# Performance work log

Hardware: AMD Instinct MI355X
Metric: run time of the kernel (lower is better)

The kernel has to match this reference:

```python
import jax, jax.numpy as jnp
import numpy as np
from jax import lax

N_FFT = 1024
HOP = 256
FFT_BIN = N_FFT // 2 + 1  # 513


def make_stft_kernel(n_fft: int) -> jnp.ndarray:
    """Fixed DFT basis kernel, shape (2*fft_bin, 1, n_fft), windowed with periodic Hann."""
    fft_bin = n_fft // 2 + 1
    # torch.linspace(0, 1, n_fft) is endpoint-inclusive, same as jnp.linspace
    t = jnp.linspace(0.0, 1.0, n_fft, dtype=jnp.float32)[None, None, :]
    k = jnp.arange(fft_bin, dtype=jnp.float32)[:, None, None]
    xt = t * k * (2.0 * jnp.pi)
    kernel = jnp.concatenate([jnp.cos(xt), jnp.sin(xt)], axis=0)  # (2*fft_bin, 1, n_fft)
    # torch.hann_window is periodic: 0.5*(1 - cos(2*pi*n/N))
    n = jnp.arange(n_fft, dtype=jnp.float32)
    hann = 0.5 * (1.0 - jnp.cos(2.0 * jnp.pi * n / n_fft))
    return kernel * hann[None, None, :]


def setup_inputs() -> dict:
    key = jax.random.key(0)
    x = jax.random.normal(key, (16, 1, 262144), dtype=jnp.float32)
    kernel = make_stft_kernel(N_FFT)
    return {"x": x, "kernel": kernel}


def reference(x, kernel):
    # padding == 'center'
    left = N_FFT // 2
    right = N_FFT - left
    x = jnp.pad(x, ((0, 0), (0, 0), (left, right)))
    # strided conv1d with fixed DFT-basis kernel
    y = lax.conv_general_dilated(
        x, kernel,
        window_strides=(HOP,),
        padding='VALID',
        dimension_numbers=('NCW', 'OIW', 'NCW'),
    )  # (B, 2*fft_bin, num_frames)
    real, imag = jnp.split(y, 2, axis=1)
    return real, imag
```

## Files before the change

### kernel.cpp

```cpp
#include <hip/hip_runtime.h>
#include <hip/hip_bf16.h>

#define NFFT    1024
#define HOPSZ   256
#define XLEN    262144
#define PADLEN  (XLEN + NFFT)
#define NBATCH  16
#define NBINS2  1026
#define FBIN    513
#define NFRAMES 1025
#define NGF     (NBATCH * NFRAMES)
#define TOTOUT  ((size_t)NBATCH * FBIN * NFRAMES)

#define KT 64
#define NKT 16
#define NT_TILES 64
#define MT_TILES 4
#define NWG (MT_TILES * NT_TILES)
#define ABYTES 32768
#define BUFE   32768
#define BUFB   65536
#define NTAIL  49184
#define PSTRIDE 132
#define LDS_BYTES (256 * PSTRIDE * 4)

typedef short bf16x8 __attribute__((ext_vector_type(8)));
typedef float f32x4  __attribute__((ext_vector_type(4)));
typedef unsigned short u16x8 __attribute__((ext_vector_type(8)));
typedef unsigned short u16x4 __attribute__((ext_vector_type(4)));

__device__ __forceinline__ unsigned short f2bf(float f) {
  union { float f; unsigned u; } v; v.f = f;
  unsigned r = v.u + 0x7fffu + ((v.u >> 16) & 1u);
  return (unsigned short)(r >> 16);
}
__device__ __forceinline__ float bf2f(unsigned short h) {
  union { unsigned u; float f; } v; v.u = ((unsigned)h) << 16; return v.f;
}

typedef __attribute__((address_space(1))) void void_g;
typedef __attribute__((address_space(3))) void void_l;
__device__ __forceinline__ void gload_lds16(const void* g, void* l) {
  __builtin_amdgcn_global_load_lds((void_g*)(g), (void_l*)(l), 16, 0, 0);
}

__global__ __launch_bounds__(256) void pack_x_kernel(const float* __restrict__ x,
                                                     unsigned short* __restrict__ xp) {
  long long t = (long long)blockIdx.x * 256 + threadIdx.x;
  long long base = t * 8;
  if (base >= (long long)NBATCH * PADLEN) return;
  int b   = (int)(base / PADLEN);
  int pos = (int)(base % PADLEN);
  const float* xb = x + (long long)b * XLEN;
  u16x8 v;
#pragma unroll
  for (int j = 0; j < 8; ++j) {
    int xi = pos + j - (NFFT / 2);
    float f = ((unsigned)xi < (unsigned)XLEN) ? xb[xi] : 0.0f;
    v[j] = f2bf(f);
  }
  *reinterpret_cast<u16x8*>(xp + base) = v;
}

__global__ __launch_bounds__(256) void pack_w_kernel(const float* __restrict__ W,
                                                     unsigned short* __restrict__ Wb) {
  long long t = ((long long)blockIdx.x * 256 + threadIdx.x) * 4;
  if (t >= (long long)NBINS2 * NFFT) return;
  float4 f = *reinterpret_cast<const float4*>(W + t);
  u16x4 v;
  v[0] = f2bf(f.x); v[1] = f2bf(f.y); v[2] = f2bf(f.z); v[3] = f2bf(f.w);
  *reinterpret_cast<u16x4*>(Wb + t) = v;
}

__global__ __launch_bounds__(512, 2) void stft_mfma8_kernel(const unsigned short* __restrict__ Xp,
                                                            const unsigned short* __restrict__ Wb,
                                                            float* __restrict__ out) {
  extern __shared__ unsigned short lds[];
  const int tid = threadIdx.x;
  const int l   = tid & 63;
  const int w   = tid >> 6;
  const int wr  = w >> 2;
  const int wc  = w & 3;
  const int r16 = l & 15, hi = l >> 4;

  const int bid = blockIdx.x;
  const int c_  = bid >> 3;
  const int nt  = (bid & 7) * 8 + (c_ & 7);
  const int mt  = c_ >> 3;
  const int bin0 = mt * 256;
  const int gf0  = nt * 256;

  const int lr = l >> 3;
  const int ls = l & 7;
  const int cswz = ((ls ^ lr) << 3);

  unsigned aqoff[4];
#pragma unroll
  for (int qi = 0; qi < 4; ++qi)
    aqoff[qi] = (unsigned)(bin0 + qi * 64 + w * 8 + lr) * NFFT + cswz;
  unsigned boff[4];
#pragma unroll
  for (int j = 0; j < 4; ++j) {
    const int gf = gf0 + (w * 4 + j) * 8 + lr;
    const int bb = gf / NFRAMES;
    const int fr = gf - bb * NFRAMES;
    boff[j] = (unsigned)bb * PADLEN + (unsigned)fr * HOPSZ + cswz;
  }

#define STAGE(D, KC) do { \
    _Pragma("unroll") \
    for (int q_ = 0; q_ < 4; ++q_) \
      gload_lds16(Wb + aqoff[q_] + (KC), lds + (D) * BUFE + q_ * 4096 + w * 512); \
    _Pragma("unroll") \
    for (int j_ = 0; j_ < 4; ++j_) \
      gload_lds16(Xp + boff[j_] + (KC), lds + (D) * BUFE + 16384 + (w * 4 + j_) * 512); \
    } while (0)

  const int aB0 = (wr * 128 + r16) * 128;
  const int bB0 = ABYTES + (wc * 64 + r16) * 128;
  const int swz = (r16 & 7) << 4;
  const int c0  = (hi * 16) ^ swz;
  const int c1  = (64 + hi * 16) ^ swz;

#define RD12(BASE, C, AARR, BARR) do { \
    _Pragma("unroll") \
    for (int n_ = 0; n_ < 4; ++n_) \
      BARR[n_] = *reinterpret_cast<const bf16x8*>((const char*)(BASE) + bB0 + n_ * 2048 + (C)); \
    _Pragma("unroll") \
    for (int m_ = 0; m_ < 8; ++m_) \
      AARR[m_] = *reinterpret_cast<const bf16x8*>((const char*)(BASE) + aB0 + m_ * 2048 + (C)); \
    } while (0)

#define MFMA32(AARR, BARR) do { \
    __builtin_amdgcn_s_setprio(1); \
    _Pragma("unroll") \
    for (int m_ = 0; m_ < 8; ++m_) { \
      _Pragma("unroll") \
      for (int n_ = 0; n_ < 4; ++n_) \
        acc[m_][n_] = __builtin_amdgcn_mfma_f32_16x16x32_bf16(AARR[m_], BARR[n_], acc[m_][n_], 0, 0, 0); \
    } \
    __builtin_amdgcn_s_setprio(0); } while (0)

  f32x4 acc[8][4] = {};
  bf16x8 A0[8], B0[4], A1[8], B1[4];

  STAGE(0, 0);
  STAGE(1, KT);
  asm volatile("s_waitcnt vmcnt(8)" ::: "memory");
  __builtin_amdgcn_s_barrier();
  __builtin_amdgcn_sched_barrier(0);
  RD12(lds, c0, A0, B0);

  for (int t = 0; t < NKT; ++t) {
    const int ci = t & 1;
    const char* cbuf = (const char*)lds + ci * BUFB;
    const char* nbuf = (const char*)lds + (ci ^ 1) * BUFB;
    const int kc2 = (t + 2) << 6;

    RD12(cbuf, c1, A1, B1);
    __builtin_amdgcn_sched_barrier(0);
    asm volatile("s_waitcnt lgkmcnt(12)" ::: "memory");
    __builtin_amdgcn_sched_barrier(0);
    MFMA32(A0, B0);

    asm volatile("s_waitcnt vmcnt(0) lgkmcnt(0)" ::: "memory");
    __builtin_amdgcn_sched_barrier(0);
    __builtin_amdgcn_s_barrier();
    __builtin_amdgcn_sched_barrier(0);
    if (t < NKT - 1) RD12(nbuf, c0, A0, B0);
    if (t < NKT - 2) STAGE(ci, kc2);
    __builtin_amdgcn_sched_barrier(0);
    MFMA32(A1, B1);
  }

  {
    float* patch = (float*)lds;
    const int col     = l & 15;
    const int rbase   = (l >> 4) * 4;
    const int h_mine  = wc >> 1;
    const int colbase = (wc & 1) * 64;

#pragma unroll
    for (int h = 0; h < 2; ++h) {
      __builtin_amdgcn_s_barrier();
      if (h_mine == h) {
#pragma unroll
        for (int m = 0; m < 8; ++m)
#pragma unroll
          for (int n2 = 0; n2 < 4; ++n2)
#pragma unroll
            for (int r = 0; r < 4; ++r)
              patch[(wr * 128 + m * 16 + rbase + r) * PSTRIDE + colbase + n2 * 16 + col] =
                  acc[m][n2][r];
      }
      __builtin_amdgcn_s_barrier();

      size_t baseR[2];
      int cols[2];
#pragma unroll
      for (int j = 0; j < 2; ++j) {
        const int gf = gf0 + h * 128 + j * 64 + l;
        const int bb = gf / NFRAMES;
        const int fr = gf - bb * NFRAMES;
        baseR[j] = (size_t)bb * FBIN * NFRAMES + fr;
        cols[j]  = j * 64 + l;
      }
      for (int i = 0; i < 32; ++i) {
        const int row = i * 8 + w;
        const int bin = bin0 + row;
        const size_t binoff = (size_t)bin * NFRAMES;
#pragma unroll
        for (int j = 0; j < 2; ++j) {
          const float v = patch[row * PSTRIDE + cols[j]];
          size_t off = binoff + (bin < FBIN ? baseR[j]
                                            : baseR[j] + TOTOUT - (size_t)FBIN * NFRAMES);
          out[off] = v;
        }
      }
    }
  }
#undef STAGE
#undef RD12
#undef MFMA32
}

__global__ __launch_bounds__(512) void stft_tail_kernel(const unsigned short* __restrict__ Xp,
                                                        const unsigned short* __restrict__ Wb,
                                                        float* __restrict__ out) {
  const int wid = (int)((blockIdx.x * 512 + threadIdx.x) >> 6);
  const int l   = threadIdx.x & 63;
  if (wid >= NTAIL) return;
  int bin, gf;
  if (wid < 2 * NGF) { bin = 1024 + (wid & 1); gf = wid >> 1; }
  else { const int s = wid - 2 * NGF; gf = 16384 + (s & 15); bin = s >> 4; }
  const int bb = gf / NFRAMES;
  const int fr = gf - bb * NFRAMES;
  const unsigned short* xr = Xp + (size_t)bb * PADLEN + (size_t)fr * HOPSZ + l * 16;
  const unsigned short* wr = Wb + (size_t)bin * NFFT + l * 16;
  u16x8 x0 = *reinterpret_cast<const u16x8*>(xr);
  u16x8 x1 = *reinterpret_cast<const u16x8*>(xr + 8);
  u16x8 w0 = *reinterpret_cast<const u16x8*>(wr);
  u16x8 w1 = *reinterpret_cast<const u16x8*>(wr + 8);
  float s0 = 0.f, s1 = 0.f;
#pragma unroll
  for (int j = 0; j < 8; ++j) {
    s0 = fmaf(bf2f(x0[j]), bf2f(w0[j]), s0);
    s1 = fmaf(bf2f(x1[j]), bf2f(w1[j]), s1);
  }
  float s = s0 + s1;
#pragma unroll
  for (int k = 32; k >= 1; k >>= 1) s += __shfl_xor(s, k);
  if (l == 0) {
    size_t off;
    if (bin < FBIN) off = ((size_t)bb * FBIN + bin) * NFRAMES + fr;
    else            off = TOTOUT + ((size_t)bb * FBIN + (bin - FBIN)) * NFRAMES + fr;
    out[off] = s;
  }
}

__global__ void stft_direct_kernel(const float* __restrict__ x, const float* __restrict__ W,
                                   float* __restrict__ out,
                                   int bin_lo, int nbins, int fr_lo, int nframes) {
  long long total = (long long)NBATCH * nbins * nframes;
  for (long long t = (long long)blockIdx.x * blockDim.x + threadIdx.x; t < total;
       t += (long long)gridDim.x * blockDim.x) {
    int fr = fr_lo + (int)(t % nframes);
    long long q = t / nframes;
    int bin = bin_lo + (int)(q % nbins);
    int b   = (int)(q / nbins);
    const float* xb = x + (long long)b * XLEN;
    const float* wrow = W + (long long)bin * NFFT;
    float s = 0.f;
    const int base = fr * HOPSZ - (NFFT / 2);
    for (int j = 0; j < NFFT; ++j) {
      int xi = base + j;
      float xv = ((unsigned)xi < (unsigned)XLEN) ? xb[xi] : 0.f;
      s = fmaf(xv, wrow[j], s);
    }
    size_t off;
    if (bin < FBIN) off = ((size_t)b * FBIN + bin) * NFRAMES + fr;
    else            off = TOTOUT + ((size_t)b * FBIN + (bin - FBIN)) * NFRAMES + fr;
    out[off] = s;
  }
}

extern "C" void kernel_launch(void* const* d_in, const int* in_sizes, int n_in,
                              void* d_out, int out_size, void* d_ws, size_t ws_size,
                              hipStream_t stream) {
  const float* x = (const float*)d_in[0];
  const float* W = (const float*)d_in[1];
  float* out = (float*)d_out;

  const size_t xp_bytes = (size_t)NBATCH * PADLEN * sizeof(unsigned short);
  const size_t wb_bytes = (size_t)NBINS2 * NFFT * sizeof(unsigned short);

  if (ws_size >= xp_bytes + wb_bytes) {
    unsigned short* xp = (unsigned short*)d_ws;
    unsigned short* wb = (unsigned short*)((char*)d_ws + xp_bytes);

    {
      long long threads = (long long)NBATCH * PADLEN / 8;
      pack_x_kernel<<<(int)((threads + 255) / 256), 256, 0, stream>>>(x, xp);
    }
    pack_w_kernel<<<(NBINS2 * NFFT / 4 + 255) / 256, 256, 0, stream>>>(W, wb);

    stft_mfma8_kernel<<<NWG, 512, LDS_BYTES, stream>>>(xp, wb, out);
    stft_tail_kernel<<<NTAIL / 8, 512, 0, stream>>>(xp, wb, out);
  } else {
    stft_direct_kernel<<<2048, 256, 0, stream>>>(x, W, out, 0, NBINS2, 0, NFRAMES);
  }
}
```

Before: 69.39 us.

## Shrink GEMM tile to 128x128 with 4 waves and merge pack kernels

```diff
diff --git a/kernel.cpp b/kernel.cpp
--- a/kernel.cpp
+++ b/kernel.cpp
@@ -14,15 +14,15 @@
 
 #define KT 64
 #define NKT 16
-#define NT_TILES 64
-#define MT_TILES 4
-#define NWG (MT_TILES * NT_TILES)
-#define ABYTES 32768
-#define BUFE   32768
-#define BUFB   65536
+#define NWG 1024
+#define BUFE 16384
+#define BUFB 32768
+#define LDS_BYTES (2 * BUFB)
 #define NTAIL  49184
 #define PSTRIDE 132
-#define LDS_BYTES (256 * PSTRIDE * 4)
+
+#define PX_BLKS 2056
+#define PW_BLKS 1026
 
 typedef short bf16x8 __attribute__((ext_vector_type(8)));
 typedef float f32x4  __attribute__((ext_vector_type(4)));
@@ -44,61 +44,61 @@
   __builtin_amdgcn_global_load_lds((void_g*)(g), (void_l*)(l), 16, 0, 0);
 }
 
-__global__ __launch_bounds__(256) void pack_x_kernel(const float* __restrict__ x,
-                                                     unsigned short* __restrict__ xp) {
-  long long t = (long long)blockIdx.x * 256 + threadIdx.x;
-  long long base = t * 8;
-  if (base >= (long long)NBATCH * PADLEN) return;
-  int b   = (int)(base / PADLEN);
-  int pos = (int)(base % PADLEN);
-  const float* xb = x + (long long)b * XLEN;
-  u16x8 v;
-#pragma unroll
-  for (int j = 0; j < 8; ++j) {
-    int xi = pos + j - (NFFT / 2);
-    float f = ((unsigned)xi < (unsigned)XLEN) ? xb[xi] : 0.0f;
-    v[j] = f2bf(f);
-  }
-  *reinterpret_cast<u16x8*>(xp + base) = v;
-}
-
-__global__ __launch_bounds__(256) void pack_w_kernel(const float* __restrict__ W,
-                                                     unsigned short* __restrict__ Wb) {
-  long long t = ((long long)blockIdx.x * 256 + threadIdx.x) * 4;
-  if (t >= (long long)NBINS2 * NFFT) return;
-  float4 f = *reinterpret_cast<const float4*>(W + t);
-  u16x4 v;
-  v[0] = f2bf(f.x); v[1] = f2bf(f.y); v[2] = f2bf(f.z); v[3] = f2bf(f.w);
-  *reinterpret_cast<u16x4*>(Wb + t) = v;
-}
-
-__global__ __launch_bounds__(512, 2) void stft_mfma8_kernel(const unsigned short* __restrict__ Xp,
-                                                            const unsigned short* __restrict__ Wb,
-                                                            float* __restrict__ out) {
+__global__ __launch_bounds__(256) void pack_kernel(const float* __restrict__ x,
+                                                   const float* __restrict__ W,
+                                                   unsigned short* __restrict__ xp,
+                                                   unsigned short* __restrict__ wb) {
+  const int bid = blockIdx.x;
+  const int tid = threadIdx.x;
+  if (bid < PX_BLKS) {
+    long long base = ((long long)bid * 256 + tid) * 8;
+    int b   = (int)(base / PADLEN);
+    int pos = (int)(base % PADLEN);
+    const float* xb = x + (long long)b * XLEN;
+    u16x8 v;
+#pragma unroll
+    for (int j = 0; j < 8; ++j) {
+      int xi = pos + j - (NFFT / 2);
+      float f = ((unsigned)xi < (unsigned)XLEN) ? xb[xi] : 0.0f;
+      v[j] = f2bf(f);
+    }
+    *reinterpret_cast<u16x8*>(xp + base) = v;
+  } else {
+    long long t = (((long long)(bid - PX_BLKS)) * 256 + tid) * 4;
+    float4 f = *reinterpret_cast<const float4*>(W + t);
+    u16x4 v;
+    v[0] = f2bf(f.x); v[1] = f2bf(f.y); v[2] = f2bf(f.z); v[3] = f2bf(f.w);
+    *reinterpret_cast<u16x4*>(wb + t) = v;
+  }
+}
+
+__global__ __launch_bounds__(256, 2) void stft_mfma128_kernel(const unsigned short* __restrict__ Xp,
+                                                              const unsigned short* __restrict__ Wb,
+                                                              float* __restrict__ out) {
   extern __shared__ unsigned short lds[];
   const int tid = threadIdx.x;
   const int l   = tid & 63;
   const int w   = tid >> 6;
-  const int wr  = w >> 2;
-  const int wc  = w & 3;
+  const int wr  = w >> 1;
+  const int wc  = w & 1;
   const int r16 = l & 15, hi = l >> 4;
 
-  const int bid = blockIdx.x;
-  const int c_  = bid >> 3;
-  const int nt  = (bid & 7) * 8 + (c_ & 7);
-  const int mt  = c_ >> 3;
-  const int bin0 = mt * 256;
-  const int gf0  = nt * 256;
+  const int bid   = blockIdx.x;
+  const int xcd   = bid & 7;
+  const int local = bid >> 3;
+  const int nt    = xcd * 16 + (local >> 3);
+  const int mt    = local & 7;
+  const int bin0  = mt * 128;
+  const int gf0   = nt * 128;
 
   const int lr = l >> 3;
   const int ls = l & 7;
   const int cswz = ((ls ^ lr) << 3);
 
-  unsigned aqoff[4];
-#pragma unroll
-  for (int qi = 0; qi < 4; ++qi)
-    aqoff[qi] = (unsigned)(bin0 + qi * 64 + w * 8 + lr) * NFFT + cswz;
-  unsigned boff[4];
+  unsigned aqoff[4], boff[4];
+#pragma unroll
+  for (int q = 0; q < 4; ++q)
+    aqoff[q] = (unsigned)(bin0 + (w * 4 + q) * 8 + lr) * NFFT + cswz;
 #pragma unroll
   for (int j = 0; j < 4; ++j) {
     const int gf = gf0 + (w * 4 + j) * 8 + lr;
@@ -110,108 +110,106 @@
 #define STAGE(D, KC) do { \
     _Pragma("unroll") \
     for (int q_ = 0; q_ < 4; ++q_) \
-      gload_lds16(Wb + aqoff[q_] + (KC), lds + (D) * BUFE + q_ * 4096 + w * 512); \
+      gload_lds16(Wb + aqoff[q_] + (KC), lds + (D) * BUFE + (w * 4 + q_) * 512); \
     _Pragma("unroll") \
     for (int j_ = 0; j_ < 4; ++j_) \
-      gload_lds16(Xp + boff[j_] + (KC), lds + (D) * BUFE + 16384 + (w * 4 + j_) * 512); \
+      gload_lds16(Xp + boff[j_] + (KC), lds + (D) * BUFE + 8192 + (w * 4 + j_) * 512); \
     } while (0)
 
-  const int aB0 = (wr * 128 + r16) * 128;
-  const int bB0 = ABYTES + (wc * 64 + r16) * 128;
+  const int aB0 = (wr * 64 + r16) * 128;
+  const int bB0 = 16384 + (wc * 64 + r16) * 128;
   const int swz = (r16 & 7) << 4;
   const int c0  = (hi * 16) ^ swz;
   const int c1  = (64 + hi * 16) ^ swz;
 
-#define RD12(BASE, C, AARR, BARR) do { \
+#define RD8(BASE, C, AARR, BARR) do { \
     _Pragma("unroll") \
     for (int n_ = 0; n_ < 4; ++n_) \
       BARR[n_] = *reinterpret_cast<const bf16x8*>((const char*)(BASE) + bB0 + n_ * 2048 + (C)); \
     _Pragma("unroll") \
-    for (int m_ = 0; m_ < 8; ++m_) \
+    for (int m_ = 0; m_ < 4; ++m_) \
       AARR[m_] = *reinterpret_cast<const bf16x8*>((const char*)(BASE) + aB0 + m_ * 2048 + (C)); \
     } while (0)
 
-#define MFMA32(AARR, BARR) do { \
+#define MFMA16(AARR, BARR) do { \
     __builtin_amdgcn_s_setprio(1); \
     _Pragma("unroll") \
-    for (int m_ = 0; m_ < 8; ++m_) { \
+    for (int m_ = 0; m_ < 4; ++m_) { \
       _Pragma("unroll") \
       for (int n_ = 0; n_ < 4; ++n_) \
         acc[m_][n_] = __builtin_amdgcn_mfma_f32_16x16x32_bf16(AARR[m_], BARR[n_], acc[m_][n_], 0, 0, 0); \
     } \
     __builtin_amdgcn_s_setprio(0); } while (0)
 
-  f32x4 acc[8][4] = {};
-  bf16x8 A0[8], B0[4], A1[8], B1[4];
+  f32x4 acc[4][4] = {};
+  bf16x8 A0[4], B0[4], A1[4], B1[4];
 
   STAGE(0, 0);
   STAGE(1, KT);
   asm volatile("s_waitcnt vmcnt(8)" ::: "memory");
   __builtin_amdgcn_s_barrier();
   __builtin_amdgcn_sched_barrier(0);
-  RD12(lds, c0, A0, B0);
-
+  RD8(lds, c0, A0, B0);
+
+#pragma unroll 1
   for (int t = 0; t < NKT; ++t) {
     const int ci = t & 1;
     const char* cbuf = (const char*)lds + ci * BUFB;
     const char* nbuf = (const char*)lds + (ci ^ 1) * BUFB;
     const int kc2 = (t + 2) << 6;
 
-    RD12(cbuf, c1, A1, B1);
-    __builtin_amdgcn_sched_barrier(0);
-    asm volatile("s_waitcnt lgkmcnt(12)" ::: "memory");
-    __builtin_amdgcn_sched_barrier(0);
-    MFMA32(A0, B0);
+    RD8(cbuf, c1, A1, B1);
+    __builtin_amdgcn_sched_barrier(0);
+    asm volatile("s_waitcnt lgkmcnt(8)" ::: "memory");
+    __builtin_amdgcn_sched_barrier(0);
+    MFMA16(A0, B0);
 
     asm volatile("s_waitcnt vmcnt(0) lgkmcnt(0)" ::: "memory");
     __builtin_amdgcn_sched_barrier(0);
     __builtin_amdgcn_s_barrier();
     __builtin_amdgcn_sched_barrier(0);
-    if (t < NKT - 1) RD12(nbuf, c0, A0, B0);
+    if (t < NKT - 1) RD8(nbuf, c0, A0, B0);
     if (t < NKT - 2) STAGE(ci, kc2);
     __builtin_amdgcn_sched_barrier(0);
-    MFMA32(A1, B1);
+    MFMA16(A1, B1);
   }
 
   {
     float* patch = (float*)lds;
-    const int col     = l & 15;
-    const int rbase   = (l >> 4) * 4;
-    const int h_mine  = wc >> 1;
-    const int colbase = (wc & 1) * 64;
-
-#pragma unroll
-    for (int h = 0; h < 2; ++h) {
+    const int col   = l & 15;
+    const int rbase = (l >> 4) * 4;
+    const int colbase = wc * 64;
+
+    size_t baseR[2];
+#pragma unroll
+    for (int j = 0; j < 2; ++j) {
+      const int gf = gf0 + j * 64 + l;
+      const int bb = gf / NFRAMES;
+      const int fr = gf - bb * NFRAMES;
+      baseR[j] = (size_t)bb * FBIN * NFRAMES + fr;
+    }
+
+#pragma unroll
+    for (int c = 0; c < 2; ++c) {
       __builtin_amdgcn_s_barrier();
-      if (h_mine == h) {
-#pragma unroll
-        for (int m = 0; m < 8; ++m)
-#pragma unroll
-          for (int n2 = 0; n2 < 4; ++n2)
+      if (wr == c) {
+#pragma unroll
+        for (int m = 0; m < 4; ++m)
+#pragma unroll
+          for (int n = 0; n < 4; ++n)
 #pragma unroll
             for (int r = 0; r < 4; ++r)
-              patch[(wr * 128 + m * 16 + rbase + r) * PSTRIDE + colbase + n2 * 16 + col] =
-                  acc[m][n2][r];
+              patch[(m * 16 + rbase + r) * PSTRIDE + colbase + n * 16 + col] = acc[m][n][r];
       }
       __builtin_amdgcn_s_barrier();
 
-      size_t baseR[2];
-      int cols[2];
-#pragma unroll
-      for (int j = 0; j < 2; ++j) {
-        const int gf = gf0 + h * 128 + j * 64 + l;
-        const int bb = gf / NFRAMES;
-        const int fr = gf - bb * NFRAMES;
-        baseR[j] = (size_t)bb * FBIN * NFRAMES + fr;
-        cols[j]  = j * 64 + l;
-      }
-      for (int i = 0; i < 32; ++i) {
-        const int row = i * 8 + w;
-        const int bin = bin0 + row;
+      for (int i = 0; i < 16; ++i) {
+        const int row = i * 4 + w;
+        const int bin = bin0 + c * 64 + row;
         const size_t binoff = (size_t)bin * NFRAMES;
 #pragma unroll
         for (int j = 0; j < 2; ++j) {
-          const float v = patch[row * PSTRIDE + cols[j]];
+          const float v = patch[row * PSTRIDE + j * 64 + l];
           size_t off = binoff + (bin < FBIN ? baseR[j]
                                             : baseR[j] + TOTOUT - (size_t)FBIN * NFRAMES);
           out[off] = v;
@@ -220,8 +218,8 @@
     }
   }
 #undef STAGE
-#undef RD12
-#undef MFMA32
+#undef RD8
+#undef MFMA16
 }
 
 __global__ __launch_bounds__(512) void stft_tail_kernel(const unsigned short* __restrict__ Xp,
@@ -298,13 +296,8 @@
     unsigned short* xp = (unsigned short*)d_ws;
     unsigned short* wb = (unsigned short*)((char*)d_ws + xp_bytes);
 
-    {
-      long long threads = (long long)NBATCH * PADLEN / 8;
-      pack_x_kernel<<<(int)((threads + 255) / 256), 256, 0, stream>>>(x, xp);
-    }
-    pack_w_kernel<<<(NBINS2 * NFFT / 4 + 255) / 256, 256, 0, stream>>>(W, wb);
-
-    stft_mfma8_kernel<<<NWG, 512, LDS_BYTES, stream>>>(xp, wb, out);
+    pack_kernel<<<PX_BLKS + PW_BLKS, 256, 0, stream>>>(x, W, xp, wb);
+    stft_mfma128_kernel<<<NWG, 256, LDS_BYTES, stream>>>(xp, wb, out);
     stft_tail_kernel<<<NTAIL / 8, 512, 0, stream>>>(xp, wb, out);
   } else {
     stft_direct_kernel<<<2048, 256, 0, stream>>>(x, W, out, 0, NBINS2, 0, NFRAMES);
```

After: 66.09 us, median of 4. 1.05x faster.
